# Optimization experiments

Hardware: AMD Instinct MI355X
Metric: run time of the kernel (lower is better)

The kernel has to match this reference:

```python
import jax, jax.numpy as jnp
import numpy as np

N = 50000
E = 800000
IN_C = 256
OUT_C = 128
HID = 2 * OUT_C  # 256


def setup_inputs() -> dict:
    key = jax.random.key(0)
    ks = jax.random.split(key, 8)
    def glorot(k, fan_in, fan_out):
        lim = (6.0 / (fan_in + fan_out)) ** 0.5
        return jax.random.uniform(k, (fan_in, fan_out), jnp.float32, -lim, lim)
    x = jax.random.normal(ks[0], (N, IN_C), dtype=jnp.float32)
    edge_index = jax.random.randint(ks[1], (2, E), 0, N, dtype=jnp.int64)
    return {
        "x": x,
        "edge_index": edge_index,
        "W1": glorot(ks[2], IN_C, HID),
        "b1": jnp.zeros((HID,), jnp.float32),
        "W_mu": glorot(ks[3], HID, OUT_C),
        "b_mu": jnp.zeros((OUT_C,), jnp.float32),
        "W_ls": glorot(ks[4], HID, OUT_C),
        "b_ls": jnp.zeros((OUT_C,), jnp.float32),
    }


def _gcn_norm(edge_index, n):
    # PyG GCNConv default: add self-loops, symmetric normalization D^-1/2 A D^-1/2
    loop = jnp.arange(n, dtype=edge_index.dtype)
    src = jnp.concatenate([edge_index[0], loop])  # [E+N]
    dst = jnp.concatenate([edge_index[1], loop])
    deg = jax.ops.segment_sum(jnp.ones_like(dst, dtype=jnp.float32), dst, num_segments=n)
    dinv = jnp.where(deg > 0, jax.lax.rsqrt(deg), 0.0)
    norm = dinv[src] * dinv[dst]  # [E+N]
    return src, dst, norm


def _gcn_conv(x, W, b, src, dst, norm, n):
    h = x @ W                                   # [N, F_out] transform first (F_out < F_in ok)
    msg = h[src] * norm[:, None]                # [E+N, F_out] gather + scale
    out = jax.ops.segment_sum(msg, dst, num_segments=n)  # scatter-add aggregate
    return out + b


def reference(x, edge_index, W1, b1, W_mu, b_mu, W_ls, b_ls):
    n = x.shape[0]
    src, dst, norm = _gcn_norm(edge_index, n)
    h = jax.nn.relu(_gcn_conv(x, W1, b1, src, dst, norm, n))
    mu = _gcn_conv(h, W_mu, b_mu, src, dst, norm, n)
    logstd = _gcn_conv(h, W_ls, b_ls, src, dst, norm, n)
    return (mu, logstd)
```

## Files before the change

kernel.cpp:

```cpp
#include <hip/hip_runtime.h>

#define NN 50000
#define EE 800000
#define NBIN 391
#define BINCAP 2560
#define NB_P1 391
#define NB_PB 256

typedef _Float16 half8 __attribute__((ext_vector_type(8)));
typedef float f32x4 __attribute__((ext_vector_type(4)));
typedef unsigned short ushort8v __attribute__((ext_vector_type(8)));
typedef unsigned short ushort4v __attribute__((ext_vector_type(4)));

__device__ __forceinline__ unsigned short f2h(float f){
  _Float16 h = (_Float16)f; unsigned short u; __builtin_memcpy(&u, &h, 2); return u;
}
__device__ __forceinline__ float h2f(unsigned short u){
  _Float16 h; __builtin_memcpy(&h, &u, 2); return (float)h;
}
__device__ __forceinline__ void split2h(float v, unsigned short* p){
  _Float16 hi = (_Float16)v;
  _Float16 lo = (_Float16)(v - (float)hi);
  __builtin_memcpy(p, &hi, 2);
  __builtin_memcpy(p+1, &lo, 2);
}
__device__ __forceinline__ void gl2lds16(const unsigned short* g, unsigned short* l){
  __builtin_amdgcn_global_load_lds(
    (const __attribute__((address_space(1))) unsigned int*)g,
    (__attribute__((address_space(3))) unsigned int*)l, 16, 0, 0);
}

__device__ __forceinline__ int detect_m(const int* eidx, int* sh){
  int t = threadIdx.x;
  if (t < 64){
    int v = eidx[2*t + 1];
    unsigned long long nz = __ballot(v != 0);
    if (t == 0) *sh = (nz == 0ULL) ? 1 : 0;
  }
  __syncthreads();
  return *sh;
}

__global__ __launch_bounds__(512) void k_prep(const int* __restrict__ eidx,
    const float* __restrict__ W1,
    const float* __restrict__ Wmu, const float* __restrict__ Wls,
    int* __restrict__ gcur, unsigned int* __restrict__ binbuf,
    unsigned short* __restrict__ Bt1, unsigned short* __restrict__ Bt2){
  int b = blockIdx.x;
  int tid = threadIdx.x;
  if (b < NB_P1){
    __shared__ int msh;
    __shared__ int hist[NBIN];
    __shared__ int base[NBIN];
    int m = detect_m(eidx, &msh);
    for (int k = tid; k < NBIN; k += 512) hist[k] = 0;
    __syncthreads();
    int sv[4], dl[4], cb[4], ofs[4];
    #pragma unroll
    for (int j = 0; j < 4; ++j){
      int e = b*2048 + j*512 + tid;
      cb[j] = -1;
      if (e < EE){
        sv[j] = m ? eidx[2*e]        : eidx[e];
        int d  = m ? eidx[2*(EE + e)] : eidx[EE + e];
        cb[j] = d >> 7; dl[j] = d & 127;
        ofs[j] = atomicAdd(&hist[cb[j]], 1);
      }
    }
    __syncthreads();
    for (int k = tid; k < NBIN; k += 512)
      base[k] = hist[k] ? atomicAdd(&gcur[k], hist[k]) : 0;
    __syncthreads();
    #pragma unroll
    for (int j = 0; j < 4; ++j){
      if (cb[j] >= 0){
        int p = base[cb[j]] + ofs[j];
        if (p < BINCAP)
          binbuf[(size_t)cb[j]*BINCAP + p] = (unsigned)sv[j] | ((unsigned)dl[j] << 16);
      }
    }
  } else {
    int gid = (b - NB_P1)*512 + tid;
    int idx = gid & 65535;
    int n = idx & 255, k = idx >> 8;
    if (gid < 65536){
      unsigned short hq = f2h(W1[k*256 + n]);
      unsigned short* p = Bt1 + (size_t)n*512 + 2*k;
      p[0] = hq; p[1] = hq;
    } else {
      float w = (n < 128) ? Wmu[k*128 + n] : Wls[k*128 + (n - 128)];
      Bt2[(size_t)n*256 + k] = f2h(w);
    }
  }
}

__global__ __launch_bounds__(512) void k_pass2(const unsigned int* __restrict__ binbuf,
    const int* __restrict__ gcur, int* __restrict__ cnt,
    unsigned short* __restrict__ bk){
  __shared__ int lcnt[128];
  __shared__ __align__(16) unsigned short lbk[128*64];
  int c = blockIdx.x;
  int tid = threadIdx.x;
  if (tid < 128) lcnt[tid] = 0;
  __syncthreads();
  int n = gcur[c]; if (n > BINCAP) n = BINCAP;
  const unsigned int* bb = binbuf + (size_t)c*BINCAP;
  for (int t = tid; t < n; t += 512){
    unsigned v = bb[t];
    int dloc = v >> 16;
    int slot = atomicAdd(&lcnt[dloc], 1);
    if (slot < 64) lbk[dloc*64 + slot] = (unsigned short)(v & 0xFFFF);
  }
  __syncthreads();
  #pragma unroll
  for (int k = 0; k < 2; ++k){
    int idx = k*512 + tid;
    int node = c*128 + (idx >> 3);
    if (node < NN)
      *(uint4*)(bk + (size_t)c*128*64 + idx*8) = *(const uint4*)(lbk + idx*8);
  }
  if (tid < 128){
    int node = c*128 + tid;
    if (node < NN) cnt[node] = lcnt[tid];
  }
}

__global__ __launch_bounds__(256, 3) void k_gemm8x(const float* __restrict__ X,
    const unsigned short* __restrict__ Bt, unsigned short* __restrict__ C,
    int M, const int* __restrict__ cnt){
  __shared__ __align__(16) unsigned short sA[128*64];
  __shared__ __align__(16) unsigned short sB[2][128*64];
  const int g = blockIdx.x;
  const int xc = g & 7, s = g >> 3;
  const int tN = s & 1;
  const int tM = (s >> 1)*8 + xc;
  const int nTM = (M + 127) >> 7;
  if (tM >= nTM) return;
  const int tid  = threadIdx.x;
  const int wave = tid >> 6, lane = tid & 63;
  const int wm = wave >> 1, wn = wave & 1;
  const int quad = lane >> 4, l16 = lane & 15;
  const int rsub = lane >> 3;
  const int l7   = lane & 7;
  const int chs  = l7 ^ rsub;

  int arow[4];
  #pragma unroll
  for (int j = 0; j < 4; ++j){
    int q = wave*4 + j, r = q*8 + rsub;
    int a = tM*128 + r; if (a >= M) a = M-1;
    arow[j] = a;
  }

  f32x4 acc[4][4] = {};

  #pragma unroll
  for (int j = 0; j < 4; ++j){
    int q = wave*4 + j, r = q*8 + rsub;
    gl2lds16(Bt + (size_t)(tN*128 + r)*512 + chs*8, &sB[0][q*512]);
  }
  __builtin_amdgcn_sched_barrier(0);
  float4 v[4];
  float4 vn[4] = {};
  #pragma unroll
  for (int j = 0; j < 4; ++j)
    v[j] = *(const float4*)(X + (size_t)arow[j]*256 + chs*4);

  #pragma unroll
  for (int kt = 0; kt < 8; ++kt){
    #pragma unroll
    for (int j = 0; j < 4; ++j){
      int q = wave*4 + j;
      __attribute__((aligned(16))) unsigned short sh[8];
      split2h(v[j].x, sh);   split2h(v[j].y, sh+2);
      split2h(v[j].z, sh+4); split2h(v[j].w, sh+6);
      *(uint4*)(&sA[q*512 + lane*8]) = *(const uint4*)(sh);
    }
    if (kt < 7){
      #pragma unroll
      for (int j = 0; j < 4; ++j){
        int q = wave*4 + j, r = q*8 + rsub;
        gl2lds16(Bt + (size_t)(tN*128 + r)*512 + (kt+1)*64 + chs*8,
                 &sB[(kt+1)&1][q*512]);
      }
      __builtin_amdgcn_sched_barrier(0);
      #pragma unroll
      for (int j = 0; j < 4; ++j)
        vn[j] = *(const float4*)(X + (size_t)arow[j]*256 + (kt+1)*32 + chs*4);
    }
    asm volatile("s_waitcnt lgkmcnt(0)" ::: "memory");
    __builtin_amdgcn_sched_barrier(0);
    __builtin_amdgcn_s_barrier();
    #pragma unroll
    for (int ks = 0; ks < 2; ++ks){
      half8 af[4], bfr[4];
      #pragma unroll
      for (int t = 0; t < 4; ++t){
        int R = wm*64 + t*16 + l16;
        af[t]  = *(const half8*)(&sA[R*64 + ((ks*4 + quad) ^ (R & 7))*8]);
      }
      #pragma unroll
      for (int t = 0; t < 4; ++t){
        int R = wn*64 + t*16 + l16;
        bfr[t] = *(const half8*)(&sB[kt & 1][R*64 + ((ks*4 + quad) ^ (R & 7))*8]);
      }
      #pragma unroll
      for (int mt = 0; mt < 4; ++mt)
        #pragma unroll
        for (int nt = 0; nt < 4; ++nt)
          acc[mt][nt] = __builtin_amdgcn_mfma_f32_16x16x32_f16(af[mt], bfr[nt], acc[mt][nt], 0, 0, 0);
    }
    asm volatile("s_waitcnt lgkmcnt(0)" ::: "memory");
    __builtin_amdgcn_sched_barrier(0);
    __builtin_amdgcn_s_barrier();
    #pragma unroll
    for (int j = 0; j < 4; ++j) v[j] = vn[j];
  }

  #pragma unroll
  for (int mt = 0; mt < 4; ++mt){
    #pragma unroll
    for (int r = 0; r < 4; ++r){
      int row = tM*128 + wm*64 + mt*16 + quad*4 + r;
      if (row < M){
        float sc = rsqrtf((float)(cnt[row] + 1));
        #pragma unroll
        for (int nt = 0; nt < 4; ++nt){
          int cc = tN*128 + wn*64 + nt*16 + l16;
          C[(size_t)row*256 + cc] = f2h(acc[mt][nt][r] * sc);
        }
      }
    }
  }
}

__global__ __launch_bounds__(256, 3) void k_gemm4p(const unsigned short* __restrict__ A,
    const unsigned short* __restrict__ Bt, unsigned short* __restrict__ C, int M){
  __shared__ __align__(16) unsigned short sA[128*64];
  __shared__ __align__(16) unsigned short sB[2][128*64];
  const int g = blockIdx.x;
  const int xc = g & 7, s = g >> 3;
  const int tN = s & 1;
  const int tM = (s >> 1)*8 + xc;
  const int nTM = (M + 127) >> 7;
  if (tM >= nTM) return;
  const int tid  = threadIdx.x;
  const int wave = tid >> 6, lane = tid & 63;
  const int wm = wave >> 1, wn = wave & 1;
  const int quad = lane >> 4, l16 = lane & 15;
  const int rsub = lane >> 3;
  const int l7   = lane & 7;
  const int chs  = l7 ^ rsub;

  int arow[4];
  #pragma unroll
  for (int j = 0; j < 4; ++j){
    int q = wave*4 + j, r = q*8 + rsub;
    int a = tM*128 + r; if (a >= M) a = M-1;
    arow[j] = a;
  }

  f32x4 acc[4][4] = {};

  #pragma unroll
  for (int j = 0; j < 4; ++j){
    int q = wave*4 + j, r = q*8 + rsub;
    gl2lds16(Bt + (size_t)(tN*128 + r)*256 + chs*8, &sB[0][q*512]);
  }
  __builtin_amdgcn_sched_barrier(0);
  uint4 av[4];
  uint4 avn[4] = {};
  #pragma unroll
  for (int j = 0; j < 4; ++j)
    av[j] = *(const uint4*)(A + (size_t)arow[j]*256 + chs*8);

  #pragma unroll
  for (int kt = 0; kt < 4; ++kt){
    #pragma unroll
    for (int j = 0; j < 4; ++j){
      int q = wave*4 + j;
      *(uint4*)(&sA[q*512 + lane*8]) = av[j];
    }
    if (kt < 3){
      #pragma unroll
      for (int j = 0; j < 4; ++j){
        int q = wave*4 + j, r = q*8 + rsub;
        gl2lds16(Bt + (size_t)(tN*128 + r)*256 + (kt+1)*64 + chs*8,
                 &sB[(kt+1)&1][q*512]);
      }
      __builtin_amdgcn_sched_barrier(0);
      #pragma unroll
      for (int j = 0; j < 4; ++j)
        avn[j] = *(const uint4*)(A + (size_t)arow[j]*256 + (kt+1)*64 + chs*8);
    }
    asm volatile("s_waitcnt lgkmcnt(0)" ::: "memory");
    __builtin_amdgcn_sched_barrier(0);
    __builtin_amdgcn_s_barrier();
    #pragma unroll
    for (int ks = 0; ks < 2; ++ks){
      half8 af[4], bfr[4];
      #pragma unroll
      for (int t = 0; t < 4; ++t){
        int R = wm*64 + t*16 + l16;
        af[t]  = *(const half8*)(&sA[R*64 + ((ks*4 + quad) ^ (R & 7))*8]);
      }
      #pragma unroll
      for (int t = 0; t < 4; ++t){
        int R = wn*64 + t*16 + l16;
        bfr[t] = *(const half8*)(&sB[kt & 1][R*64 + ((ks*4 + quad) ^ (R & 7))*8]);
      }
      #pragma unroll
      for (int mt = 0; mt < 4; ++mt)
        #pragma unroll
        for (int nt = 0; nt < 4; ++nt)
          acc[mt][nt] = __builtin_amdgcn_mfma_f32_16x16x32_f16(af[mt], bfr[nt], acc[mt][nt], 0, 0, 0);
    }
    asm volatile("s_waitcnt lgkmcnt(0)" ::: "memory");
    __builtin_amdgcn_sched_barrier(0);
    __builtin_amdgcn_s_barrier();
    #pragma unroll
    for (int j = 0; j < 4; ++j) av[j] = avn[j];
  }

  #pragma unroll
  for (int mt = 0; mt < 4; ++mt){
    #pragma unroll
    for (int r = 0; r < 4; ++r){
      int row = tM*128 + wm*64 + mt*16 + quad*4 + r;
      if (row < M){
        #pragma unroll
        for (int nt = 0; nt < 4; ++nt){
          int cc = tN*128 + wn*64 + nt*16 + l16;
          C[(size_t)row*256 + cc] = f2h(acc[mt][nt][r]);
        }
      }
    }
  }
}

__global__ __launch_bounds__(256) void k_agg_relu(const unsigned short* __restrict__ feat,
    const int* __restrict__ cnt, const unsigned short* __restrict__ bkall,
    const float* __restrict__ b1, unsigned short* __restrict__ h1){
  int i = blockIdx.x*4 + (threadIdx.x >> 6);
  int lane = threadIdx.x & 63;
  int f0 = lane*4;
  int deg = cnt[i]; if (deg > 64) deg = 64;
  float di = rsqrtf((float)(deg + 1));
  const unsigned short* bk = bkall + ((size_t)i << 6);
  ushort4 hv = *(const ushort4*)(feat + (size_t)i*256 + f0);
  float p0 = h2f(hv.x), p1 = h2f(hv.y), p2 = h2f(hv.z), p3 = h2f(hv.w);
  float q0=0.f,q1=0.f,q2=0.f,q3=0.f, r0=0.f,r1=0.f,r2=0.f,r3=0.f, t0=0.f,t1=0.f,t2=0.f,t3=0.f;
  int e = 0;
  for (; e + 8 <= deg; e += 8){
    ushort8v sa = *(const ushort8v*)(bk + e);
    ushort4 v0 = *(const ushort4*)(feat + (size_t)sa[0]*256 + f0);
    ushort4 v1 = *(const ushort4*)(feat + (size_t)sa[1]*256 + f0);
    ushort4 v2 = *(const ushort4*)(feat + (size_t)sa[2]*256 + f0);
    ushort4 v3 = *(const ushort4*)(feat + (size_t)sa[3]*256 + f0);
    ushort4 v4 = *(const ushort4*)(feat + (size_t)sa[4]*256 + f0);
    ushort4 v5 = *(const ushort4*)(feat + (size_t)sa[5]*256 + f0);
    ushort4 v6 = *(const ushort4*)(feat + (size_t)sa[6]*256 + f0);
    ushort4 v7 = *(const ushort4*)(feat + (size_t)sa[7]*256 + f0);
    p0 += h2f(v0.x); p1 += h2f(v0.y); p2 += h2f(v0.z); p3 += h2f(v0.w);
    q0 += h2f(v1.x); q1 += h2f(v1.y); q2 += h2f(v1.z); q3 += h2f(v1.w);
    r0 += h2f(v2.x); r1 += h2f(v2.y); r2 += h2f(v2.z); r3 += h2f(v2.w);
    t0 += h2f(v3.x); t1 += h2f(v3.y); t2 += h2f(v3.z); t3 += h2f(v3.w);
    p0 += h2f(v4.x); p1 += h2f(v4.y); p2 += h2f(v4.z); p3 += h2f(v4.w);
    q0 += h2f(v5.x); q1 += h2f(v5.y); q2 += h2f(v5.z); q3 += h2f(v5.w);
    r0 += h2f(v6.x); r1 += h2f(v6.y); r2 += h2f(v6.z); r3 += h2f(v6.w);
    t0 += h2f(v7.x); t1 += h2f(v7.y); t2 += h2f(v7.z); t3 += h2f(v7.w);
  }
  if (e + 4 <= deg){
    ushort4v sa = *(const ushort4v*)(bk + e);
    ushort4 v0 = *(const ushort4*)(feat + (size_t)sa[0]*256 + f0);
    ushort4 v1 = *(const ushort4*)(feat + (size_t)sa[1]*256 + f0);
    ushort4 v2 = *(const ushort4*)(feat + (size_t)sa[2]*256 + f0);
    ushort4 v3 = *(const ushort4*)(feat + (size_t)sa[3]*256 + f0);
    p0 += h2f(v0.x); p1 += h2f(v0.y); p2 += h2f(v0.z); p3 += h2f(v0.w);
    q0 += h2f(v1.x); q1 += h2f(v1.y); q2 += h2f(v1.z); q3 += h2f(v1.w);
    r0 += h2f(v2.x); r1 += h2f(v2.y); r2 += h2f(v2.z); r3 += h2f(v2.w);
    t0 += h2f(v3.x); t1 += h2f(v3.y); t2 += h2f(v3.z); t3 += h2f(v3.w);
    e += 4;
  }
  for (; e < deg; ++e){
    int s = bk[e];
    ushort4 v = *(const ushort4*)(feat + (size_t)s*256 + f0);
    p0 += h2f(v.x); p1 += h2f(v.y); p2 += h2f(v.z); p3 += h2f(v.w);
  }
  float s0 = p0+q0+r0+t0, s1 = p1+q1+r1+t1, s2 = p2+q2+r2+t2, s3 = p3+q3+r3+t3;
  float4 bb = *(const float4*)(b1 + f0);
  float u0 = fmaxf(di*s0 + bb.x, 0.f);
  float u1 = fmaxf(di*s1 + bb.y, 0.f);
  float u2 = fmaxf(di*s2 + bb.z, 0.f);
  float u3 = fmaxf(di*s3 + bb.w, 0.f);
  ushort4 o;
  o.x = f2h(di*u0); o.y = f2h(di*u1); o.z = f2h(di*u2); o.w = f2h(di*u3);
  *(ushort4*)(h1 + (size_t)i*256 + f0) = o;
}

__global__ __launch_bounds__(256) void k_agg_out(const unsigned short* __restrict__ feat,
    const int* __restrict__ cnt, const unsigned short* __restrict__ bkall,
    const float* __restrict__ bmu, const float* __restrict__ bls, float* __restrict__ outp){
  int i = blockIdx.x*4 + (threadIdx.x >> 6);
  int lane = threadIdx.x & 63;
  int f0 = lane*4;
  int deg = cnt[i]; if (deg > 64) deg = 64;
  float di = rsqrtf((float)(deg + 1));
  const unsigned short* bk = bkall + ((size_t)i << 6);
  ushort4 hv = *(const ushort4*)(feat + (size_t)i*256 + f0);
  float p0 = h2f(hv.x), p1 = h2f(hv.y), p2 = h2f(hv.z), p3 = h2f(hv.w);
  float q0=0.f,q1=0.f,q2=0.f,q3=0.f, r0=0.f,r1=0.f,r2=0.f,r3=0.f, t0=0.f,t1=0.f,t2=0.f,t3=0.f;
  int e = 0;
  for (; e + 8 <= deg; e += 8){
    ushort8v sa = *(const ushort8v*)(bk + e);
    ushort4 v0 = *(const ushort4*)(feat + (size_t)sa[0]*256 + f0);
    ushort4 v1 = *(const ushort4*)(feat + (size_t)sa[1]*256 + f0);
    ushort4 v2 = *(const ushort4*)(feat + (size_t)sa[2]*256 + f0);
    ushort4 v3 = *(const ushort4*)(feat + (size_t)sa[3]*256 + f0);
    ushort4 v4 = *(const ushort4*)(feat + (size_t)sa[4]*256 + f0);
    ushort4 v5 = *(const ushort4*)(feat + (size_t)sa[5]*256 + f0);
    ushort4 v6 = *(const ushort4*)(feat + (size_t)sa[6]*256 + f0);
    ushort4 v7 = *(const ushort4*)(feat + (size_t)sa[7]*256 + f0);
    p0 += h2f(v0.x); p1 += h2f(v0.y); p2 += h2f(v0.z); p3 += h2f(v0.w);
    q0 += h2f(v1.x); q1 += h2f(v1.y); q2 += h2f(v1.z); q3 += h2f(v1.w);
    r0 += h2f(v2.x); r1 += h2f(v2.y); r2 += h2f(v2.z); r3 += h2f(v2.w);
    t0 += h2f(v3.x); t1 += h2f(v3.y); t2 += h2f(v3.z); t3 += h2f(v3.w);
    p0 += h2f(v4.x); p1 += h2f(v4.y); p2 += h2f(v4.z); p3 += h2f(v4.w);
    q0 += h2f(v5.x); q1 += h2f(v5.y); q2 += h2f(v5.z); q3 += h2f(v5.w);
    r0 += h2f(v6.x); r1 += h2f(v6.y); r2 += h2f(v6.z); r3 += h2f(v6.w);
    t0 += h2f(v7.x); t1 += h2f(v7.y); t2 += h2f(v7.z); t3 += h2f(v7.w);
  }
  if (e + 4 <= deg){
    ushort4v sa = *(const ushort4v*)(bk + e);
    ushort4 v0 = *(const ushort4*)(feat + (size_t)sa[0]*256 + f0);
    ushort4 v1 = *(const ushort4*)(feat + (size_t)sa[1]*256 + f0);
    ushort4 v2 = *(const ushort4*)(feat + (size_t)sa[2]*256 + f0);
    ushort4 v3 = *(const ushort4*)(feat + (size_t)sa[3]*256 + f0);
    p0 += h2f(v0.x); p1 += h2f(v0.y); p2 += h2f(v0.z); p3 += h2f(v0.w);
    q0 += h2f(v1.x); q1 += h2f(v1.y); q2 += h2f(v1.z); q3 += h2f(v1.w);
    r0 += h2f(v2.x); r1 += h2f(v2.y); r2 += h2f(v2.z); r3 += h2f(v2.w);
    t0 += h2f(v3.x); t1 += h2f(v3.y); t2 += h2f(v3.z); t3 += h2f(v3.w);
    e += 4;
  }
  for (; e < deg; ++e){
    int s = bk[e];
    ushort4 v = *(const ushort4*)(feat + (size_t)s*256 + f0);
    p0 += h2f(v.x); p1 += h2f(v.y); p2 += h2f(v.z); p3 += h2f(v.w);
  }
  float a0 = di*(p0+q0+r0+t0), a1 = di*(p1+q1+r1+t1);
  float a2 = di*(p2+q2+r2+t2), a3 = di*(p3+q3+r3+t3);
  float4 o;
  if (f0 < 128){
    float4 bb = *(const float4*)(bmu + f0);
    o.x = a0 + bb.x; o.y = a1 + bb.y; o.z = a2 + bb.z; o.w = a3 + bb.w;
    *(float4*)(outp + (size_t)i*128 + f0) = o;
  } else {
    int g = f0 - 128;
    float4 bb = *(const float4*)(bls + g);
    o.x = a0 + bb.x; o.y = a1 + bb.y; o.z = a2 + bb.z; o.w = a3 + bb.w;
    *(float4*)(outp + (size_t)NN*128 + (size_t)i*128 + g) = o;
  }
}

extern "C" void kernel_launch(void* const* d_in, const int* in_sizes, int n_in,
                              void* d_out, int out_size, void* d_ws, size_t ws_size,
                              hipStream_t stream){
  const float* x   = (const float*)d_in[0];
  const int* eidx  = (const int*)d_in[1];
  const float* W1  = (const float*)d_in[2];
  const float* b1  = (const float*)d_in[3];
  const float* Wmu = (const float*)d_in[4];
  const float* bmu = (const float*)d_in[5];
  const float* Wls = (const float*)d_in[6];
  const float* bls = (const float*)d_in[7];
  float* out = (float*)d_out;

  char* ws = (char*)d_ws;
  size_t off = 0;
  auto alloc = [&](size_t bytes)->char*{
    char* p = ws + off; off = (off + bytes + 511) & ~(size_t)511; return p;
  };
  int* gcur     = (int*)alloc(NBIN*4);
  unsigned int* binbuf = (unsigned int*)alloc((size_t)NBIN*BINCAP*4);
  int* cnt      = (int*)alloc(NN*4);
  unsigned short* buckets = (unsigned short*)alloc((size_t)NN*64*2);
  unsigned short* Bt1 = (unsigned short*)alloc((size_t)256*512*2);
  unsigned short* Bt2 = (unsigned short*)alloc((size_t)256*256*2);
  unsigned short* h1  = (unsigned short*)alloc((size_t)NN*256*2);
  unsigned short* h   = (unsigned short*)alloc((size_t)NN*256*2);
  unsigned short* z   = h;

  hipMemsetAsync(gcur, 0, NBIN*4, stream);
  k_prep<<<NB_P1 + NB_PB, 512, 0, stream>>>(eidx, W1, Wmu, Wls,
                                            gcur, binbuf, Bt1, Bt2);
  k_pass2<<<NBIN, 512, 0, stream>>>(binbuf, gcur, cnt, buckets);
  k_gemm8x<<<784, 256, 0, stream>>>(x, Bt1, h, NN, cnt);
  k_agg_relu<<<12500, 256, 0, stream>>>(h, cnt, buckets, b1, h1);
  k_gemm4p<<<784, 256, 0, stream>>>(h1, Bt2, z, NN);
  k_agg_out<<<12500, 256, 0, stream>>>(z, cnt, buckets, bmu, bls, out);
}
```

Measured before the change: 291.2 us.

## Fold bucket-fill pass into GEMM launch and compute degrees via global atomics

Removes the separate k_pass2 launch by appending its per-bin bucket-fill work as extra blocks of the first GEMM kernel, reusing the GEMM's shared-memory buffers. Per-node in-degree counts are now accumulated with global atomics in k_prep, and the memset is widened to zero the count array too. This saves one kernel launch and lets the bucketing overlap the GEMM, at the cost of 800k global atomics and larger GEMM-kernel blocks for the bucket work.

```diff
diff --git a/kernel.cpp b/kernel.cpp
--- a/kernel.cpp
+++ b/kernel.cpp
@@ -45,7 +45,8 @@
     const float* __restrict__ W1,
     const float* __restrict__ Wmu, const float* __restrict__ Wls,
     int* __restrict__ gcur, unsigned int* __restrict__ binbuf,
-    unsigned short* __restrict__ Bt1, unsigned short* __restrict__ Bt2){
+    unsigned short* __restrict__ Bt1, unsigned short* __restrict__ Bt2,
+    int* __restrict__ cnt){
   int b = blockIdx.x;
   int tid = threadIdx.x;
   if (b < NB_P1){
@@ -64,6 +65,7 @@
         sv[j] = m ? eidx[2*e]        : eidx[e];
         int d  = m ? eidx[2*(EE + e)] : eidx[EE + e];
         cb[j] = d >> 7; dl[j] = d & 127;
+        atomicAdd(&cnt[d], 1);
         ofs[j] = atomicAdd(&hist[cb[j]], 1);
       }
     }
@@ -94,49 +96,44 @@
   }
 }
 
-__global__ __launch_bounds__(512) void k_pass2(const unsigned int* __restrict__ binbuf,
-    const int* __restrict__ gcur, int* __restrict__ cnt,
-    unsigned short* __restrict__ bk){
-  __shared__ int lcnt[128];
-  __shared__ __align__(16) unsigned short lbk[128*64];
-  int c = blockIdx.x;
-  int tid = threadIdx.x;
-  if (tid < 128) lcnt[tid] = 0;
-  __syncthreads();
-  int n = gcur[c]; if (n > BINCAP) n = BINCAP;
-  const unsigned int* bb = binbuf + (size_t)c*BINCAP;
-  for (int t = tid; t < n; t += 512){
-    unsigned v = bb[t];
-    int dloc = v >> 16;
-    int slot = atomicAdd(&lcnt[dloc], 1);
-    if (slot < 64) lbk[dloc*64 + slot] = (unsigned short)(v & 0xFFFF);
-  }
-  __syncthreads();
-  #pragma unroll
-  for (int k = 0; k < 2; ++k){
-    int idx = k*512 + tid;
-    int node = c*128 + (idx >> 3);
-    if (node < NN)
-      *(uint4*)(bk + (size_t)c*128*64 + idx*8) = *(const uint4*)(lbk + idx*8);
-  }
-  if (tid < 128){
-    int node = c*128 + tid;
-    if (node < NN) cnt[node] = lcnt[tid];
-  }
-}
-
 __global__ __launch_bounds__(256, 3) void k_gemm8x(const float* __restrict__ X,
     const unsigned short* __restrict__ Bt, unsigned short* __restrict__ C,
-    int M, const int* __restrict__ cnt){
+    int M, const int* __restrict__ cnt,
+    const unsigned int* __restrict__ binbuf, const int* __restrict__ gcur,
+    unsigned short* __restrict__ bk){
   __shared__ __align__(16) unsigned short sA[128*64];
   __shared__ __align__(16) unsigned short sB[2][128*64];
   const int g = blockIdx.x;
+  const int tid  = threadIdx.x;
+  if (g >= 784){
+    int c = g - 784;
+    int* lcnt = (int*)sB;
+    unsigned short* lbk = sA;
+    if (tid < 128) lcnt[tid] = 0;
+    __syncthreads();
+    int n = gcur[c]; if (n > BINCAP) n = BINCAP;
+    const unsigned int* bb = binbuf + (size_t)c*BINCAP;
+    for (int t = tid; t < n; t += 256){
+      unsigned v = bb[t];
+      int dloc = v >> 16;
+      int slot = atomicAdd(&lcnt[dloc], 1);
+      if (slot < 64) lbk[dloc*64 + slot] = (unsigned short)(v & 0xFFFF);
+    }
+    __syncthreads();
+    #pragma unroll
+    for (int k = 0; k < 4; ++k){
+      int idx = k*256 + tid;
+      int node = c*128 + (idx >> 3);
+      if (node < NN)
+        *(uint4*)(bk + (size_t)c*128*64 + idx*8) = *(const uint4*)(lbk + idx*8);
+    }
+    return;
+  }
   const int xc = g & 7, s = g >> 3;
   const int tN = s & 1;
   const int tM = (s >> 1)*8 + xc;
   const int nTM = (M + 127) >> 7;
   if (tM >= nTM) return;
-  const int tid  = threadIdx.x;
   const int wave = tid >> 6, lane = tid & 63;
   const int wm = wave >> 1, wn = wave & 1;
   const int quad = lane >> 4, l16 = lane & 15;
@@ -481,8 +478,9 @@
     char* p = ws + off; off = (off + bytes + 511) & ~(size_t)511; return p;
   };
   int* gcur     = (int*)alloc(NBIN*4);
+  int* cnt      = (int*)alloc(NN*4);
+  size_t zero_span = (size_t)((char*)cnt - (char*)gcur) + NN*4;
   unsigned int* binbuf = (unsigned int*)alloc((size_t)NBIN*BINCAP*4);
-  int* cnt      = (int*)alloc(NN*4);
   unsigned short* buckets = (unsigned short*)alloc((size_t)NN*64*2);
   unsigned short* Bt1 = (unsigned short*)alloc((size_t)256*512*2);
   unsigned short* Bt2 = (unsigned short*)alloc((size_t)256*256*2);
@@ -490,11 +488,11 @@
   unsigned short* h   = (unsigned short*)alloc((size_t)NN*256*2);
   unsigned short* z   = h;
 
-  hipMemsetAsync(gcur, 0, NBIN*4, stream);
+  hipMemsetAsync(gcur, 0, zero_span, stream);
   k_prep<<<NB_P1 + NB_PB, 512, 0, stream>>>(eidx, W1, Wmu, Wls,
-                                            gcur, binbuf, Bt1, Bt2);
-  k_pass2<<<NBIN, 512, 0, stream>>>(binbuf, gcur, cnt, buckets);
-  k_gemm8x<<<784, 256, 0, stream>>>(x, Bt1, h, NN, cnt);
+                                            gcur, binbuf, Bt1, Bt2, cnt);
+  k_gemm8x<<<784 + NBIN, 256, 0, stream>>>(x, Bt1, h, NN, cnt,
+                                           binbuf, gcur, buckets);
   k_agg_relu<<<12500, 256, 0, stream>>>(h, cnt, buckets, b1, h1);
   k_gemm4p<<<784, 256, 0, stream>>>(h1, Bt2, z, NN);
   k_agg_out<<<12500, 256, 0, stream>>>(z, cnt, buckets, bmu, bls, out);
```

Result: slower. 309.6 us (+6.3%).
